# Performance work log

Hardware: AMD Instinct MI355X
Metric: run time of the kernel (lower is better)

Reference implementation:

```python
import jax, jax.numpy as jnp
import numpy as np

C_IN = 256
C_INTER = 128
B, H, W = 8, 64, 64
EPS = 1e-5


def setup_inputs() -> dict:
    key = jax.random.key(0)
    ks = jax.random.split(key, 12)
    s = 0.02
    return {
        "x": jax.random.normal(ks[0], (B, C_IN, H, W), dtype=jnp.float32),
        "bn_gamma": jnp.ones((C_IN,), jnp.float32),
        "bn_beta": jnp.zeros((C_IN,), jnp.float32),
        "bn_mean": jax.random.normal(ks[1], (C_IN,), jnp.float32) * 0.1,
        "bn_var": jnp.abs(jax.random.normal(ks[2], (C_IN,), jnp.float32)) * 0.1 + 1.0,
        "w_g": jax.random.normal(ks[3], (C_INTER, C_IN), jnp.float32) * s,
        "b_g": jnp.zeros((C_INTER,), jnp.float32),
        "w_theta": jax.random.normal(ks[4], (C_INTER, C_IN), jnp.float32) * s,
        "b_theta": jnp.zeros((C_INTER,), jnp.float32),
        "w_phi": jax.random.normal(ks[5], (C_INTER, C_IN), jnp.float32) * s,
        "b_phi": jnp.zeros((C_INTER,), jnp.float32),
        "w_w": jax.random.normal(ks[6], (C_IN, C_INTER), jnp.float32) * s,
        "b_w": jnp.zeros((C_IN,), jnp.float32),
    }


def reference(x, bn_gamma, bn_beta, bn_mean, bn_var,
              w_g, b_g, w_theta, b_theta, w_phi, b_phi, w_w, b_w):
    b, c, h, w = x.shape
    # BatchNorm2d (inference form, running stats) -- self.bn in the original
    scale = bn_gamma * jax.lax.rsqrt(bn_var + EPS)
    xb = x * scale[None, :, None, None] + (bn_beta - bn_mean * scale)[None, :, None, None]
    xf = xb.reshape(b, c, h * w)  # (B, C, N); conv1x1 == channel matmul
    g = jnp.einsum('oc,bcn->bon', w_g, xf) + b_g[None, :, None]          # (B, Ci, N)
    th = jnp.einsum('oc,bcn->bon', w_theta, xf) + b_theta[None, :, None]  # (B, Ci, N)
    ph = jnp.einsum('oc,bcn->bon', w_phi, xf) + b_phi[None, :, None]      # (B, Ci, N)
    f = jnp.einsum('bcn,bcm->bnm', th, ph)  # (B, N, N), NO 1/sqrt(d) scaling
    a = jax.nn.softmax(f, axis=-1)
    y = jnp.einsum('bnm,bcm->bcn', a, g)    # (B, Ci, N)
    wy = jnp.einsum('oc,bcn->bon', w_w, y) + b_w[None, :, None]  # (B, C, N)
    return wy.reshape(b, c, h, w) + x
```

## Files before the change

kernel.cpp:

```cpp
#include <hip/hip_runtime.h>
#include <hip/hip_bf16.h>
#include <stdint.h>

#define BB   8
#define CIN  256
#define CI   128
#define NN   4096
#define EPSV 1e-5f
#define LOG2E 1.44269504088896340736f

typedef __attribute__((ext_vector_type(8))) short bf16x8;
typedef __attribute__((ext_vector_type(4))) short bf16x4;
typedef __attribute__((ext_vector_type(4))) float f32x4;
typedef __attribute__((ext_vector_type(2))) float f32x2;
typedef __attribute__((ext_vector_type(2))) unsigned int u32x2;
typedef __attribute__((ext_vector_type(4))) int i32x4;
typedef __attribute__((ext_vector_type(8))) int i32x8;

static __device__ inline short f2bf(float f) {
    uint32_t u = __builtin_bit_cast(uint32_t, f);
    u += 0x7FFFu + ((u >> 16) & 1u);
    return (short)(u >> 16);
}

static __device__ inline float bf2f(short s) {
    uint32_t u = ((uint32_t)(uint16_t)s) << 16;
    return __builtin_bit_cast(float, u);
}

static __device__ inline uint32_t cvt_pk_bf16(float lo, float hi) {
    uint32_t r;
    asm("v_cvt_pk_bf16_f32 %0, %1, %2" : "=v"(r) : "v"(lo), "v"(hi));
    return r;
}

__global__ __launch_bounds__(256) void prep_kernel(
    const float* __restrict__ wth, const float* __restrict__ wph,
    const float* __restrict__ wg,  const float* __restrict__ ww,
    short* __restrict__ wq, short* __restrict__ wwb)
{
    int t = blockIdx.x * 256 + threadIdx.x;
    if (t < 12288) {
        int s  = t >> 12;
        int r  = t & 4095;
        int o  = r >> 5;
        int j  = r & 31;
        int k  = j >> 3, jj = j & 7;
        const float* W = (s == 0) ? wth : (s == 1) ? wph : wg;
        float sc = (s == 0) ? LOG2E : 1.0f;
        const float* src = &W[(size_t)o * CIN + k * 64 + jj * 8];
        bf16x8 d;
        #pragma unroll
        for (int i = 0; i < 8; ++i) d[i] = f2bf(src[i] * sc);
        size_t doff = (size_t)s * 65536 + (size_t)k * 16384
                    + (size_t)o * 128 + (size_t)((jj ^ (o & 7)) << 4);
        *(bf16x8*)((char*)wq + doff) = d;
    } else if (t < 16384) {
        int r = t - 12288;
        int o = r >> 4, j = r & 15;
        const float* src = &ww[(size_t)o * CI + j * 8];
        bf16x8 d;
        #pragma unroll
        for (int i = 0; i < 8; ++i) d[i] = f2bf(src[i]);
        *(bf16x8*)&wwb[(size_t)o * CI + j * 8] = d;
    }
}

__global__ __launch_bounds__(256, 2) void proj_kernel(
    const float* __restrict__ x,
    const float* __restrict__ gamma, const float* __restrict__ beta,
    const float* __restrict__ mean,  const float* __restrict__ var,
    const short* __restrict__ wq,
    const float* __restrict__ bth, const float* __restrict__ bph,
    const float* __restrict__ bg,
    unsigned char* __restrict__ qp, unsigned char* __restrict__ kp,
    unsigned char* __restrict__ vt8)
{
    __shared__ float s_scale[CIN];
    __shared__ float s_shift[CIN];
    __shared__ __align__(16) short A_lds[64][264];
    __shared__ __align__(16) char  B_sh[2][128 * 128];

    const int tid = threadIdx.x;
    const int b   = blockIdx.x & 7;
    const int n0  = (blockIdx.x >> 3) * 64;
    const int w = tid >> 6, lane = tid & 63, lr = lane & 15, lg = lane >> 4;

    {
        float sc = gamma[tid] * rsqrtf(var[tid] + EPSV);
        s_scale[tid] = sc;
        s_shift[tid] = beta[tid] - mean[tid] * sc;
    }
    __syncthreads();

    #pragma unroll
    for (int p = 0; p < 8; ++p) {
        int c2 = p * 32 + (tid >> 4) * 2;
        int n4 = (tid & 15) * 4;
        f32x4 v0 = *(const f32x4*)&x[((size_t)b * CIN + c2) * NN + n0 + n4];
        f32x4 v1 = *(const f32x4*)&x[((size_t)b * CIN + c2 + 1) * NN + n0 + n4];
        float sc0 = s_scale[c2],     sh0 = s_shift[c2];
        float sc1 = s_scale[c2 + 1], sh1 = s_shift[c2 + 1];
        #pragma unroll
        for (int i = 0; i < 4; ++i) {
            uint32_t pk = cvt_pk_bf16(v0[i] * sc0 + sh0, v1[i] * sc1 + sh1);
            *(uint32_t*)&A_lds[n4 + i][c2] = pk;
        }
    }

    auto stageB = [&](int buf, int idx) {
        const char* src = (const char*)wq + (size_t)idx * 16384;
        #pragma unroll
        for (int r = 0; r < 4; ++r) {
            __builtin_amdgcn_global_load_lds(
                (const __attribute__((address_space(1))) void*)
                    (src + ((((r * 4 + w) << 6) + lane) << 4)),
                (__attribute__((address_space(3))) void*)&B_sh[buf][(r * 4 + w) << 10],
                16, 0, 0);
        }
    };
    stageB(0, 0);
    __syncthreads();

    const float* BS[3] = {bth, bph, bg};
    f32x4 acc[8];

    for (int idx = 0; idx < 12; ++idx) {
        const int s = idx >> 2, k = idx & 3, buf = idx & 1;
        if (idx + 1 < 12) stageB(buf ^ 1, idx + 1);

        if (k == 0) {
            #pragma unroll
            for (int i = 0; i < 8; ++i) acc[i] = (f32x4){0.f, 0.f, 0.f, 0.f};
        }
        const int c0 = k * 64;
        bf16x8 a0 = *(const bf16x8*)&A_lds[w * 16 + lr][c0 + lg * 8];
        bf16x8 a1 = *(const bf16x8*)&A_lds[w * 16 + lr][c0 + 32 + lg * 8];
        const char* Bc = B_sh[buf];
        #pragma unroll
        for (int ot = 0; ot < 8; ++ot) {
            const int o  = ot * 16 + lr;
            const int sw = (o & 7) << 4;
            bf16x8 b0 = *(const bf16x8*)(Bc + o * 128 + ((lg << 4) ^ sw));
            bf16x8 b1 = *(const bf16x8*)(Bc + o * 128 + (((4 + lg) << 4) ^ sw));
            acc[ot] = __builtin_amdgcn_mfma_f32_16x16x32_bf16(a0, b0, acc[ot], 0, 0, 0);
            acc[ot] = __builtin_amdgcn_mfma_f32_16x16x32_bf16(a1, b1, acc[ot], 0, 0, 0);
        }

        if (k == 3) {
            if (s < 2) {
                unsigned char* dst = (s == 0) ? qp : kp;
                const float om = (s == 0) ? LOG2E : 1.0f;
                #pragma unroll
                for (int ot = 0; ot < 8; ++ot) {
                    float bias = BS[s][ot * 16 + lr] * om;
                    #pragma unroll
                    for (int rr = 0; rr < 4; ++rr) {
                        int n = n0 + w * 16 + lg * 4 + rr;
                        uint32_t pk = __builtin_amdgcn_cvt_pk_fp8_f32(
                            acc[ot][rr] + bias, 0.f, 0, false);
                        dst[((size_t)b * NN + n) * 128 + ot * 16 + lr] =
                            (unsigned char)(pk & 0xFF);
                    }
                }
            } else {
                #pragma unroll
                for (int ot = 0; ot < 8; ++ot) {
                    float bias = BS[s][ot * 16 + lr];
                    uint32_t d = __builtin_amdgcn_cvt_pk_fp8_f32(
                        acc[ot][0] + bias, acc[ot][1] + bias, 0, false);
                    d = __builtin_amdgcn_cvt_pk_fp8_f32(
                        acc[ot][2] + bias, acc[ot][3] + bias, d, true);
                    *(uint32_t*)&vt8[((size_t)b * CI + ot * 16 + lr) * NN
                                     + n0 + w * 16 + lg * 4] = d;
                }
            }
        }
        __syncthreads();
    }
}

__global__ __launch_bounds__(256, 2) void attn_kernel(
    const unsigned char* __restrict__ qp, const unsigned char* __restrict__ kp,
    const unsigned char* __restrict__ vt8, short* __restrict__ yh,
    float* __restrict__ ml)
{
    __shared__ __align__(16) char K_sh[2][64 * 128];
    __shared__ __align__(16) char V_sh[2][128 * 128];
    __shared__ __align__(16) char P_sh[4][2][16 * 128];

    const int tid  = threadIdx.x;
    const int b    = blockIdx.x & 7;
    const int half = (blockIdx.x >> 3) & 1;
    const int n0   = (blockIdx.x >> 4) * 128;
    const int w = tid >> 6, lane = tid & 63, lr = lane & 15, lg = lane >> 4;
    const int NT = NN / 128;
    const int t0 = half * NT;

    const unsigned char* kgp[2];
    const unsigned char* vgp[4];
    #pragma unroll
    for (int r = 0; r < 2; ++r) {
        int idx = ((r * 4 + w) << 6) + lane;
        int mm  = idx >> 3, cb = (idx & 7) << 4;
        kgp[r] = kp + (size_t)b * NN * 128 + (size_t)(t0 * 64 + mm) * 128
               + (cb ^ ((mm & 7) << 4));
    }
    #pragma unroll
    for (int r = 0; r < 4; ++r) {
        int idx = ((r * 4 + w) << 6) + lane;
        int cc = idx >> 3, cbv = (idx & 7) << 4;
        vgp[r] = vt8 + (size_t)b * CI * NN + (size_t)cc * NN + t0 * 64
               + (cbv ^ ((cc & 7) << 4));
    }
    auto stageK = [&](int bufi) {
        #pragma unroll
        for (int r = 0; r < 2; ++r) {
            __builtin_amdgcn_global_load_lds(
                (const __attribute__((address_space(1))) void*)kgp[r],
                (__attribute__((address_space(3))) void*)&K_sh[bufi][(r * 4 + w) << 10],
                16, 0, 0);
            kgp[r] += 64 * 128;
        }
    };
    auto stageV = [&](int bufi) {
        #pragma unroll
        for (int r = 0; r < 4; ++r) {
            __builtin_amdgcn_global_load_lds(
                (const __attribute__((address_space(1))) void*)vgp[r],
                (__attribute__((address_space(3))) void*)&V_sh[bufi][(r * 4 + w) << 10],
                16, 0, 0);
            vgp[r] += 128;
        }
    };

    i32x8 qf8[2];
    #pragma unroll
    for (int s = 0; s < 2; ++s) {
        const unsigned char* qrow = qp + ((size_t)b * NN + n0 + w * 32 + s * 16 + lr) * 128;
        i32x4 lo = *(const i32x4*)(qrow + lg * 32);
        i32x4 hi = *(const i32x4*)(qrow + lg * 32 + 16);
        qf8[s] = (i32x8){lo[0], lo[1], lo[2], lo[3], hi[0], hi[1], hi[2], hi[3]};
    }

    f32x4 yacc[2][8];
    #pragma unroll
    for (int s = 0; s < 2; ++s)
        #pragma unroll
        for (int i = 0; i < 8; ++i) yacc[s][i] = (f32x4){0.f, 0.f, 0.f, 0.f};
    float m_run[2] = {-__builtin_huge_valf(), -__builtin_huge_valf()};
    float l_run[2] = {0.f, 0.f};

    stageK(0);
    stageV(0);
    __syncthreads();

    const int psw = (lr & 7) << 4;

    for (int t = 0; t < NT; ++t) {
        const int kcur = t & 1;
        if (t + 1 < NT) stageK(kcur ^ 1);
        const int p = t >> 1;
        if ((t & 1) == 0 && p + 1 < NT / 2) stageV((p & 1) ^ 1);

        const char* Kc = K_sh[kcur];
        f32x4 sa[2][4];
        __builtin_amdgcn_s_setprio(1);
        #pragma unroll
        for (int mt = 0; mt < 4; ++mt) {
            const int mrow = mt * 16 + lr;
            const int sw   = (mrow & 7) << 4;
            const char* kr = Kc + mrow * 128;
            i32x4 k0 = *(const i32x4*)(kr + ((lg * 32) ^ sw));
            i32x4 k1 = *(const i32x4*)(kr + ((lg * 32 + 16) ^ sw));
            i32x8 kf8 = (i32x8){k0[0], k0[1], k0[2], k0[3], k1[0], k1[1], k1[2], k1[3]};
            sa[0][mt] = __builtin_amdgcn_mfma_scale_f32_16x16x128_f8f6f4(
                kf8, qf8[0], (f32x4){0.f, 0.f, 0.f, 0.f},
                0, 0, 0, 0x7F7F7F7F, 0, 0x7F7F7F7F);
            sa[1][mt] = __builtin_amdgcn_mfma_scale_f32_16x16x128_f8f6f4(
                kf8, qf8[1], (f32x4){0.f, 0.f, 0.f, 0.f},
                0, 0, 0, 0x7F7F7F7F, 0, 0x7F7F7F7F);
        }
        __builtin_amdgcn_s_setprio(0);

        if ((t & 1) == 0) {
            float tml[2];
            #pragma unroll
            for (int s = 0; s < 2; ++s) {
                float tm = fmaxf(fmaxf(fmaxf(sa[s][0][0], sa[s][0][1]), fmaxf(sa[s][0][2], sa[s][0][3])),
                                 fmaxf(fmaxf(sa[s][1][0], sa[s][1][1]), fmaxf(sa[s][1][2], sa[s][1][3])));
                tm = fmaxf(tm, fmaxf(fmaxf(fmaxf(sa[s][2][0], sa[s][2][1]), fmaxf(sa[s][2][2], sa[s][2][3])),
                                     fmaxf(fmaxf(sa[s][3][0], sa[s][3][1]), fmaxf(sa[s][3][2], sa[s][3][3]))));
                tml[s] = tm;
            }
            if (__any((tml[0] - m_run[0] > 4.f) || (tml[1] - m_run[1] > 4.f))) {
                #pragma unroll
                for (int s = 0; s < 2; ++s) {
                    float tm = tml[s];
                    tm = fmaxf(tm, __shfl_xor(tm, 16));
                    tm = fmaxf(tm, __shfl_xor(tm, 32));
                    float mnew = fmaxf(m_run[s], tm);
                    float sc   = __builtin_amdgcn_exp2f(m_run[s] - mnew);
                    m_run[s] = mnew;
                    l_run[s] *= sc;
                    #pragma unroll
                    for (int rr = 0; rr < 4; ++rr) {
                        float scb = __shfl(sc, (lane & 48) | (lg * 4 + rr));
                        #pragma unroll
                        for (int ct = 0; ct < 8; ++ct) yacc[s][ct][rr] *= scb;
                    }
                }
            }
        }

        const int h64 = (t & 1) << 6;
        #pragma unroll
        for (int s = 0; s < 2; ++s) {
            char* Pb = &P_sh[w][s][0] + lr * 128;
            float rs = 0.f;
            #pragma unroll
            for (int mt = 0; mt < 4; ++mt) {
                float e0 = __builtin_amdgcn_exp2f(sa[s][mt][0] - m_run[s]);
                float e1 = __builtin_amdgcn_exp2f(sa[s][mt][1] - m_run[s]);
                float e2 = __builtin_amdgcn_exp2f(sa[s][mt][2] - m_run[s]);
                float e3 = __builtin_amdgcn_exp2f(sa[s][mt][3] - m_run[s]);
                rs += (e0 + e1) + (e2 + e3);
                uint32_t d = __builtin_amdgcn_cvt_pk_fp8_f32(e0, e1, 0, false);
                d = __builtin_amdgcn_cvt_pk_fp8_f32(e2, e3, d, true);
                *(uint32_t*)(Pb + ((h64 + mt * 16 + lg * 4) ^ psw)) = d;
            }
            l_run[s] += rs;
        }

        if (t & 1) {
            asm volatile("" ::: "memory");
            i32x8 pa8[2];
            #pragma unroll
            for (int s = 0; s < 2; ++s) {
                const char* Pb = &P_sh[w][s][0] + lr * 128;
                i32x4 p0 = *(const i32x4*)(Pb + ((lg * 32) ^ psw));
                i32x4 p1 = *(const i32x4*)(Pb + ((lg * 32 + 16) ^ psw));
                pa8[s] = (i32x8){p0[0], p0[1], p0[2], p0[3], p1[0], p1[1], p1[2], p1[3]};
            }
            const char* Vc = V_sh[p & 1];
            __builtin_amdgcn_s_setprio(1);
            #pragma unroll
            for (int ct = 0; ct < 8; ++ct) {
                const char* vrow = Vc + (ct * 16 + lr) * 128;
                i32x4 v0 = *(const i32x4*)(vrow + ((lg * 32) ^ psw));
                i32x4 v1 = *(const i32x4*)(vrow + ((lg * 32 + 16) ^ psw));
                i32x8 vf8 = (i32x8){v0[0], v0[1], v0[2], v0[3], v1[0], v1[1], v1[2], v1[3]};
                yacc[0][ct] = __builtin_amdgcn_mfma_scale_f32_16x16x128_f8f6f4(
                    pa8[0], vf8, yacc[0][ct], 0, 0, 0, 0x7F7F7F7F, 0, 0x7F7F7F7F);
                yacc[1][ct] = __builtin_amdgcn_mfma_scale_f32_16x16x128_f8f6f4(
                    pa8[1], vf8, yacc[1][ct], 0, 0, 0, 0x7F7F7F7F, 0, 0x7F7F7F7F);
            }
            __builtin_amdgcn_s_setprio(0);
        }

        __syncthreads();
    }

    #pragma unroll
    for (int s = 0; s < 2; ++s) {
        float lt = l_run[s];
        lt += __shfl_xor(lt, 16);
        lt += __shfl_xor(lt, 32);
        l_run[s] = lt;
    }

    short* yb = yh + ((size_t)half * BB + b) * NN * (size_t)CI;
    #pragma unroll
    for (int s = 0; s < 2; ++s) {
        #pragma unroll
        for (int rr = 0; rr < 4; ++rr) {
            int n = n0 + w * 32 + s * 16 + lg * 4 + rr;
            #pragma unroll
            for (int ct = 0; ct < 8; ++ct)
                yb[(size_t)n * CI + ct * 16 + lr] = f2bf(yacc[s][ct][rr]);
        }
    }
    if (lg == 0) {
        #pragma unroll
        for (int s = 0; s < 2; ++s) {
            int n = n0 + w * 32 + s * 16 + lr;
            f32x2 v = {m_run[s], l_run[s]};
            *(f32x2*)&ml[(((size_t)half * BB + b) * NN + n) * 2] = v;
        }
    }
}

__global__ __launch_bounds__(256) void merge_kernel(
    const short* __restrict__ yh, const float* __restrict__ ml,
    short* __restrict__ yp)
{
    const int tid = threadIdx.x;
    const int row = blockIdx.x * 8 + (tid >> 5);
    const int c4  = (tid & 31) * 4;
    const size_t H = (size_t)BB * NN * CI;
    const size_t R = (size_t)BB * NN * 2;

    float m0 = ml[(size_t)row * 2],     l0 = ml[(size_t)row * 2 + 1];
    float m1 = ml[R + (size_t)row * 2], l1 = ml[R + (size_t)row * 2 + 1];
    float mm = fmaxf(m0, m1);
    float w0 = __builtin_amdgcn_exp2f(m0 - mm);
    float w1 = __builtin_amdgcn_exp2f(m1 - mm);
    float inv = 1.0f / (l0 * w0 + l1 * w1);
    w0 *= inv; w1 *= inv;

    bf16x4 a  = *(const bf16x4*)&yh[(size_t)row * CI + c4];
    bf16x4 bb = *(const bf16x4*)&yh[H + (size_t)row * CI + c4];
    bf16x4 o;
    #pragma unroll
    for (int i = 0; i < 4; ++i) o[i] = f2bf(bf2f(a[i]) * w0 + bf2f(bb[i]) * w1);
    *(bf16x4*)&yp[(size_t)row * CI + c4] = o;
}

template <int MERGED>
__global__ __launch_bounds__(256) void out_kernel(
    const short* __restrict__ ysrc, const float* __restrict__ ml,
    const short* __restrict__ wwb, const float* __restrict__ bw,
    const float* __restrict__ x, float* __restrict__ out)
{
    __shared__ __align__(16) short A_lds[128][136];
    __shared__ __align__(16) short Bl[128][136];

    const int tid  = threadIdx.x;
    const int b    = blockIdx.x & 7;
    const int rest = blockIdx.x >> 3;
    const int ob   = rest & 1;
    const int nn   = (rest >> 1) * 128;
    const int o0   = ob * 128;
    const int w = tid >> 6, lane = tid & 63, lr = lane & 15, lg = lane >> 4;

    #pragma unroll
    for (int pass = 0; pass < 8; ++pass) {
        int o  = pass * 16 + (tid >> 4);
        int c8 = (tid & 15) * 8;
        *(bf16x8*)&A_lds[o][c8] = *(const bf16x8*)&wwb[(size_t)(o0 + o) * CI + c8];
    }
    #pragma unroll
    for (int pass = 0; pass < 8; ++pass) {
        int n  = pass * 16 + (tid >> 4);
        int c8 = (tid & 15) * 8;
        size_t row = (size_t)b * NN + nn + n;
        if (MERGED) {
            *(bf16x8*)&Bl[n][c8] = *(const bf16x8*)&ysrc[row * CI + c8];
        } else {
            const size_t H = (size_t)BB * NN * CI;
            const size_t R = (size_t)BB * NN * 2;
            f32x2 v0 = *(const f32x2*)&ml[row * 2];
            f32x2 v1 = *(const f32x2*)&ml[R + row * 2];
            float mm = fmaxf(v0[0], v1[0]);
            float w0 = __builtin_amdgcn_exp2f(v0[0] - mm);
            float w1 = __builtin_amdgcn_exp2f(v1[0] - mm);
            float inv = 1.0f / (v0[1] * w0 + v1[1] * w1);
            w0 *= inv; w1 *= inv;
            bf16x8 a  = *(const bf16x8*)&ysrc[row * CI + c8];
            bf16x8 b2 = *(const bf16x8*)&ysrc[H + row * CI + c8];
            bf16x8 ov;
            #pragma unroll
            for (int i = 0; i < 4; ++i) {
                float lo = bf2f(a[2*i]) * w0 + bf2f(b2[2*i]) * w1;
                float hi = bf2f(a[2*i+1]) * w0 + bf2f(b2[2*i+1]) * w1;
                uint32_t pk = cvt_pk_bf16(lo, hi);
                ov[2*i]   = (short)(pk & 0xFFFF);
                ov[2*i+1] = (short)(pk >> 16);
            }
            *(bf16x8*)&Bl[n][c8] = ov;
        }
    }
    __syncthreads();

    f32x4 acc[2][8];
    #pragma unroll
    for (int i = 0; i < 2; ++i)
        #pragma unroll
        for (int j = 0; j < 8; ++j) acc[i][j] = (f32x4){0.f, 0.f, 0.f, 0.f};

    #pragma unroll
    for (int kf = 0; kf < 4; ++kf) {
        bf16x8 a0 = *(const bf16x8*)&A_lds[w * 32 + lr][kf * 32 + lg * 8];
        bf16x8 a1 = *(const bf16x8*)&A_lds[w * 32 + 16 + lr][kf * 32 + lg * 8];
        #pragma unroll
        for (int nt = 0; nt < 8; ++nt) {
            bf16x8 bv = *(const bf16x8*)&Bl[nt * 16 + lr][kf * 32 + lg * 8];
            acc[0][nt] = __builtin_amdgcn_mfma_f32_16x16x32_bf16(a0, bv, acc[0][nt], 0, 0, 0);
            acc[1][nt] = __builtin_amdgcn_mfma_f32_16x16x32_bf16(a1, bv, acc[1][nt], 0, 0, 0);
        }
    }

    #pragma unroll
    for (int wo = 0; wo < 2; ++wo) {
        #pragma unroll
        for (int rr = 0; rr < 4; ++rr) {
            int o = o0 + w * 32 + wo * 16 + lg * 4 + rr;
            float bias = bw[o];
            #pragma unroll
            for (int nt = 0; nt < 8; ++nt) {
                size_t idx = ((size_t)b * CIN + o) * NN + nn + nt * 16 + lr;
                out[idx] = acc[wo][nt][rr] + bias + x[idx];
            }
        }
    }
}

extern "C" void kernel_launch(void* const* d_in, const int* in_sizes, int n_in,
                              void* d_out, int out_size, void* d_ws, size_t ws_size,
                              hipStream_t stream)
{
    const float* x     = (const float*)d_in[0];
    const float* gamma = (const float*)d_in[1];
    const float* beta  = (const float*)d_in[2];
    const float* mean  = (const float*)d_in[3];
    const float* var   = (const float*)d_in[4];
    const float* wg    = (const float*)d_in[5];
    const float* bg    = (const float*)d_in[6];
    const float* wth   = (const float*)d_in[7];
    const float* bth   = (const float*)d_in[8];
    const float* wph   = (const float*)d_in[9];
    const float* bph   = (const float*)d_in[10];
    const float* ww    = (const float*)d_in[11];
    const float* bw    = (const float*)d_in[12];

    const size_t seg = (size_t)BB * NN * CI;
    unsigned char* qp  = (unsigned char*)d_ws;
    unsigned char* kp  = (unsigned char*)d_ws + seg * sizeof(short);
    unsigned char* vt8 = (unsigned char*)d_ws + 2 * seg * sizeof(short);
    float* ml  = (float*)((char*)d_ws + 3 * seg * sizeof(short));
    short* wq  = (short*)((char*)d_ws + 25690112);
    short* wwb = (short*)((char*)d_ws + 25690112 + 196608);
    const size_t yh_off = 25u * 1024 * 1024;
    const bool fused = ws_size >= yh_off + 2 * seg * sizeof(short);
    short* yh = fused ? (short*)((char*)d_ws + yh_off) : (short*)d_out;
    (void)in_sizes; (void)n_in; (void)out_size;

    prep_kernel<<<64, 256, 0, stream>>>(wth, wph, wg, ww, wq, wwb);
    proj_kernel<<<BB * (NN / 64), 256, 0, stream>>>(
        x, gamma, beta, mean, var, wq, bth, bph, bg, qp, kp, vt8);
    attn_kernel<<<2 * BB * (NN / 128), 256, 0, stream>>>(qp, kp, vt8, yh, ml);
    if (fused) {
        out_kernel<0><<<2 * BB * (NN / 128), 256, 0, stream>>>(
            yh, ml, wwb, bw, x, (float*)d_out);
    } else {
        short* yp = (short*)d_ws;
        merge_kernel<<<BB * NN / 8, 256, 0, stream>>>(yh, ml, yp);
        out_kernel<1><<<2 * BB * (NN / 128), 256, 0, stream>>>(
            yp, ml, wwb, bw, x, (float*)d_out);
    }
}
```

Measured before the change: 100.8 us.

## Process 128-key tiles per iteration and unify K/V staging in attention loop

Measured after the change: 93.20 us (median of 2 runs). 7.6% less time.

```diff
diff --git a/kernel.cpp b/kernel.cpp
--- a/kernel.cpp
+++ b/kernel.cpp
@@ -185,47 +185,38 @@
     const unsigned char* __restrict__ vt8, short* __restrict__ yh,
     float* __restrict__ ml)
 {
-    __shared__ __align__(16) char K_sh[2][64 * 128];
+    __shared__ __align__(16) char K_sh[2][128 * 128];
     __shared__ __align__(16) char V_sh[2][128 * 128];
-    __shared__ __align__(16) char P_sh[4][2][16 * 128];
+    __shared__ __align__(16) char P_sh[4][16 * 128];
 
     const int tid  = threadIdx.x;
     const int b    = blockIdx.x & 7;
     const int half = (blockIdx.x >> 3) & 1;
     const int n0   = (blockIdx.x >> 4) * 128;
     const int w = tid >> 6, lane = tid & 63, lr = lane & 15, lg = lane >> 4;
-    const int NT = NN / 128;
+    const int NT = NN / 256;
     const int t0 = half * NT;
 
-    const unsigned char* kgp[2];
+    const unsigned char* kgp[4];
     const unsigned char* vgp[4];
     #pragma unroll
-    for (int r = 0; r < 2; ++r) {
+    for (int r = 0; r < 4; ++r) {
         int idx = ((r * 4 + w) << 6) + lane;
         int mm  = idx >> 3, cb = (idx & 7) << 4;
-        kgp[r] = kp + (size_t)b * NN * 128 + (size_t)(t0 * 64 + mm) * 128
+        kgp[r] = kp + (size_t)b * NN * 128 + (size_t)(t0 * 128 + mm) * 128
                + (cb ^ ((mm & 7) << 4));
-    }
-    #pragma unroll
-    for (int r = 0; r < 4; ++r) {
-        int idx = ((r * 4 + w) << 6) + lane;
         int cc = idx >> 3, cbv = (idx & 7) << 4;
-        vgp[r] = vt8 + (size_t)b * CI * NN + (size_t)cc * NN + t0 * 64
+        vgp[r] = vt8 + (size_t)b * CI * NN + (size_t)cc * NN + t0 * 128
                + (cbv ^ ((cc & 7) << 4));
     }
-    auto stageK = [&](int bufi) {
-        #pragma unroll
-        for (int r = 0; r < 2; ++r) {
+    auto stage = [&](int bufi) {
+        #pragma unroll
+        for (int r = 0; r < 4; ++r) {
             __builtin_amdgcn_global_load_lds(
                 (const __attribute__((address_space(1))) void*)kgp[r],
                 (__attribute__((address_space(3))) void*)&K_sh[bufi][(r * 4 + w) << 10],
                 16, 0, 0);
-            kgp[r] += 64 * 128;
-        }
-    };
-    auto stageV = [&](int bufi) {
-        #pragma unroll
-        for (int r = 0; r < 4; ++r) {
+            kgp[r] += 128 * 128;
             __builtin_amdgcn_global_load_lds(
                 (const __attribute__((address_space(1))) void*)vgp[r],
                 (__attribute__((address_space(3))) void*)&V_sh[bufi][(r * 4 + w) << 10],
@@ -251,23 +242,20 @@
     float m_run[2] = {-__builtin_huge_valf(), -__builtin_huge_valf()};
     float l_run[2] = {0.f, 0.f};
 
-    stageK(0);
-    stageV(0);
+    stage(0);
     __syncthreads();
 
     const int psw = (lr & 7) << 4;
 
     for (int t = 0; t < NT; ++t) {
-        const int kcur = t & 1;
-        if (t + 1 < NT) stageK(kcur ^ 1);
-        const int p = t >> 1;
-        if ((t & 1) == 0 && p + 1 < NT / 2) stageV((p & 1) ^ 1);
-
-        const char* Kc = K_sh[kcur];
-        f32x4 sa[2][4];
+        const int cur = t & 1;
+        if (t + 1 < NT) stage(cur ^ 1);
+
+        const char* Kc = K_sh[cur];
+        f32x4 sa[2][8];
         __builtin_amdgcn_s_setprio(1);
         #pragma unroll
-        for (int mt = 0; mt < 4; ++mt) {
+        for (int mt = 0; mt < 8; ++mt) {
             const int mrow = mt * 16 + lr;
             const int sw   = (mrow & 7) << 4;
             const char* kr = Kc + mrow * 128;
@@ -283,43 +271,42 @@
         }
         __builtin_amdgcn_s_setprio(0);
 
-        if ((t & 1) == 0) {
-            float tml[2];
+        float tml[2];
+        #pragma unroll
+        for (int s = 0; s < 2; ++s) {
+            float tm = -__builtin_huge_valf();
+            #pragma unroll
+            for (int mt = 0; mt < 8; ++mt)
+                tm = fmaxf(tm, fmaxf(fmaxf(sa[s][mt][0], sa[s][mt][1]),
+                                     fmaxf(sa[s][mt][2], sa[s][mt][3])));
+            tml[s] = tm;
+        }
+        if (__any((tml[0] - m_run[0] > 4.f) || (tml[1] - m_run[1] > 4.f))) {
             #pragma unroll
             for (int s = 0; s < 2; ++s) {
-                float tm = fmaxf(fmaxf(fmaxf(sa[s][0][0], sa[s][0][1]), fmaxf(sa[s][0][2], sa[s][0][3])),
-                                 fmaxf(fmaxf(sa[s][1][0], sa[s][1][1]), fmaxf(sa[s][1][2], sa[s][1][3])));
-                tm = fmaxf(tm, fmaxf(fmaxf(fmaxf(sa[s][2][0], sa[s][2][1]), fmaxf(sa[s][2][2], sa[s][2][3])),
-                                     fmaxf(fmaxf(sa[s][3][0], sa[s][3][1]), fmaxf(sa[s][3][2], sa[s][3][3]))));
-                tml[s] = tm;
-            }
-            if (__any((tml[0] - m_run[0] > 4.f) || (tml[1] - m_run[1] > 4.f))) {
+                float tm = tml[s];
+                tm = fmaxf(tm, __shfl_xor(tm, 16));
+                tm = fmaxf(tm, __shfl_xor(tm, 32));
+                float mnew = fmaxf(m_run[s], tm);
+                float sc   = __builtin_amdgcn_exp2f(m_run[s] - mnew);
+                m_run[s] = mnew;
+                l_run[s] *= sc;
                 #pragma unroll
-                for (int s = 0; s < 2; ++s) {
-                    float tm = tml[s];
-                    tm = fmaxf(tm, __shfl_xor(tm, 16));
-                    tm = fmaxf(tm, __shfl_xor(tm, 32));
-                    float mnew = fmaxf(m_run[s], tm);
-                    float sc   = __builtin_amdgcn_exp2f(m_run[s] - mnew);
-                    m_run[s] = mnew;
-                    l_run[s] *= sc;
+                for (int rr = 0; rr < 4; ++rr) {
+                    float scb = __shfl(sc, (lane & 48) | (lg * 4 + rr));
                     #pragma unroll
-                    for (int rr = 0; rr < 4; ++rr) {
-                        float scb = __shfl(sc, (lane & 48) | (lg * 4 + rr));
-                        #pragma unroll
-                        for (int ct = 0; ct < 8; ++ct) yacc[s][ct][rr] *= scb;
-                    }
+                    for (int ct = 0; ct < 8; ++ct) yacc[s][ct][rr] *= scb;
                 }
             }
         }
 
-        const int h64 = (t & 1) << 6;
+        i32x8 pa8[2];
         #pragma unroll
         for (int s = 0; s < 2; ++s) {
-            char* Pb = &P_sh[w][s][0] + lr * 128;
+            char* Pb = P_sh[w] + lr * 128;
             float rs = 0.f;
             #pragma unroll
-            for (int mt = 0; mt < 4; ++mt) {
+            for (int mt = 0; mt < 8; ++mt) {
                 float e0 = __builtin_amdgcn_exp2f(sa[s][mt][0] - m_run[s]);
                 float e1 = __builtin_amdgcn_exp2f(sa[s][mt][1] - m_run[s]);
                 float e2 = __builtin_amdgcn_exp2f(sa[s][mt][2] - m_run[s]);
@@ -327,36 +314,30 @@
                 rs += (e0 + e1) + (e2 + e3);
                 uint32_t d = __builtin_amdgcn_cvt_pk_fp8_f32(e0, e1, 0, false);
                 d = __builtin_amdgcn_cvt_pk_fp8_f32(e2, e3, d, true);
-                *(uint32_t*)(Pb + ((h64 + mt * 16 + lg * 4) ^ psw)) = d;
+                *(uint32_t*)(Pb + ((mt * 16 + lg * 4) ^ psw)) = d;
             }
             l_run[s] += rs;
-        }
-
-        if (t & 1) {
             asm volatile("" ::: "memory");
-            i32x8 pa8[2];
-            #pragma unroll
-            for (int s = 0; s < 2; ++s) {
-                const char* Pb = &P_sh[w][s][0] + lr * 128;
-                i32x4 p0 = *(const i32x4*)(Pb + ((lg * 32) ^ psw));
-                i32x4 p1 = *(const i32x4*)(Pb + ((lg * 32 + 16) ^ psw));
-                pa8[s] = (i32x8){p0[0], p0[1], p0[2], p0[3], p1[0], p1[1], p1[2], p1[3]};
-            }
-            const char* Vc = V_sh[p & 1];
-            __builtin_amdgcn_s_setprio(1);
-            #pragma unroll
-            for (int ct = 0; ct < 8; ++ct) {
-                const char* vrow = Vc + (ct * 16 + lr) * 128;
-                i32x4 v0 = *(const i32x4*)(vrow + ((lg * 32) ^ psw));
-                i32x4 v1 = *(const i32x4*)(vrow + ((lg * 32 + 16) ^ psw));
-                i32x8 vf8 = (i32x8){v0[0], v0[1], v0[2], v0[3], v1[0], v1[1], v1[2], v1[3]};
-                yacc[0][ct] = __builtin_amdgcn_mfma_scale_f32_16x16x128_f8f6f4(
-                    pa8[0], vf8, yacc[0][ct], 0, 0, 0, 0x7F7F7F7F, 0, 0x7F7F7F7F);
-                yacc[1][ct] = __builtin_amdgcn_mfma_scale_f32_16x16x128_f8f6f4(
-                    pa8[1], vf8, yacc[1][ct], 0, 0, 0, 0x7F7F7F7F, 0, 0x7F7F7F7F);
-            }
-            __builtin_amdgcn_s_setprio(0);
-        }
+            i32x4 p0 = *(const i32x4*)(Pb + ((lg * 32) ^ psw));
+            i32x4 p1 = *(const i32x4*)(Pb + ((lg * 32 + 16) ^ psw));
+            pa8[s] = (i32x8){p0[0], p0[1], p0[2], p0[3], p1[0], p1[1], p1[2], p1[3]};
+            asm volatile("" ::: "memory");
+        }
+
+        const char* Vc = V_sh[cur];
+        __builtin_amdgcn_s_setprio(1);
+        #pragma unroll
+        for (int ct = 0; ct < 8; ++ct) {
+            const char* vrow = Vc + (ct * 16 + lr) * 128;
+            i32x4 v0 = *(const i32x4*)(vrow + ((lg * 32) ^ psw));
+            i32x4 v1 = *(const i32x4*)(vrow + ((lg * 32 + 16) ^ psw));
+            i32x8 vf8 = (i32x8){v0[0], v0[1], v0[2], v0[3], v1[0], v1[1], v1[2], v1[3]};
+            yacc[0][ct] = __builtin_amdgcn_mfma_scale_f32_16x16x128_f8f6f4(
+                pa8[0], vf8, yacc[0][ct], 0, 0, 0, 0x7F7F7F7F, 0, 0x7F7F7F7F);
+            yacc[1][ct] = __builtin_amdgcn_mfma_scale_f32_16x16x128_f8f6f4(
+                pa8[1], vf8, yacc[1][ct], 0, 0, 0, 0x7F7F7F7F, 0, 0x7F7F7F7F);
+        }
+        __builtin_amdgcn_s_setprio(0);
 
         __syncthreads();
     }
```
